# Kernel optimization log

Measured on AMD Instinct MI355X. Metric: run time of the kernel, lower is better.

Reference implementation:

```python
import jax, jax.numpy as jnp
import numpy as np

EMBED = 1024
HEADS = 16
HEAD_DIM = EMBED // HEADS


def setup_inputs() -> dict:
    key = jax.random.key(0)
    k1, k2, k3, k4, k5 = jax.random.split(key, 5)
    x = jax.random.normal(k1, (2, 2048, EMBED), dtype=jnp.float32)
    # torch nn.Linear params: weight [out, in], bias [out]; y = x @ W.T + b
    s_attn = 1.0 / np.sqrt(EMBED)
    w_attn = jax.random.uniform(k2, (3 * EMBED, EMBED), jnp.float32, -s_attn, s_attn)
    b_attn = jax.random.uniform(k3, (3 * EMBED,), jnp.float32, -s_attn, s_attn)
    w_proj = jax.random.uniform(k4, (EMBED, EMBED), jnp.float32, -s_attn, s_attn)
    b_proj = jax.random.uniform(k5, (EMBED,), jnp.float32, -s_attn, s_attn)
    return {"x": x, "w_attn": w_attn, "b_attn": b_attn, "w_proj": w_proj, "b_proj": b_proj}


def reference(x, w_attn, b_attn, w_proj, b_proj):
    B, S, D = x.shape
    qkv = x @ w_attn.T + b_attn                      # [B, S, 3D]
    q, k, v = jnp.split(qkv, 3, axis=-1)             # each [B, S, D]

    def heads(t):  # [B, S, D] -> [B, H, S, hd]
        return t.reshape(B, S, HEADS, HEAD_DIM).transpose(0, 2, 1, 3)

    q, k, v = heads(q), heads(k), heads(v)
    # Faithful to source: NO 1/sqrt(d) scaling, NO causal mask.
    w = jnp.einsum('bhqd,bhkd->bhqk', q, k)          # [B, H, S, S]
    w = jax.nn.softmax(w, axis=-1)
    a = jnp.einsum('bhqk,bhkd->bhqd', w, v)          # [B, H, S, hd]
    a = a.transpose(0, 2, 1, 3).reshape(B, S, D)     # merge heads
    return a @ w_proj.T + b_proj
```

## Files before the change

kernel.cpp:

```cpp
#include <hip/hip_runtime.h>
#include <hip/hip_bf16.h>
#include <stdint.h>
#include <math.h>


typedef __attribute__((ext_vector_type(2))) float f32x2;
typedef __attribute__((ext_vector_type(4))) float f32x4;
typedef __attribute__((ext_vector_type(16))) float f32x16;
typedef __attribute__((ext_vector_type(8))) short bf16x8;

static __device__ __forceinline__ unsigned short f2bf(float f) {
    unsigned u = __float_as_uint(f);
    u += 0x7FFFu + ((u >> 16) & 1u);
    return (unsigned short)(u >> 16);
}
static __device__ __forceinline__ unsigned cvt_pk_bf16(float a, float b) {
    unsigned r;
    asm("v_cvt_pk_bf16_f32 %0, %1, %2" : "=v"(r) : "v"(a), "v"(b));
    return r;
}

typedef const __attribute__((address_space(1))) unsigned int* gas_ptr;
typedef __attribute__((address_space(3))) unsigned int* las_ptr;
static __device__ __forceinline__ void gload_lds16(const void* g, void* l) {
    __builtin_amdgcn_global_load_lds((gas_ptr)g, (las_ptr)l, 16, 0, 0);
}

__global__ void conv_all_kernel(const float* __restrict__ x,
                                const float* __restrict__ wa,
                                const float* __restrict__ wp,
                                unsigned short* __restrict__ x1,
                                unsigned short* __restrict__ w1a,
                                unsigned short* __restrict__ wpb) {
    int i = blockIdx.x * blockDim.x + threadIdx.x;
    int stride = gridDim.x * blockDim.x;
    for (; i < 2097152; i += stride) {
        const float* s; unsigned short* d; int j;
        if (i < 1048576)      { s = x;  d = x1;  j = i; }
        else if (i < 1835008) { s = wa; d = w1a; j = i - 1048576; }
        else                  { s = wp; d = wpb; j = i - 1835008; }
        float4 v = ((const float4*)s)[j];
        ushort4 o;
        o.x = f2bf(v.x); o.y = f2bf(v.y); o.z = f2bf(v.z); o.w = f2bf(v.w);
        ((ushort4*)d)[j] = o;
    }
}

template <int MODE>
__global__ __launch_bounds__(256, 2) void gemm_bt_kernel(
    const unsigned short* __restrict__ A,
    const unsigned short* __restrict__ Bw,
    const float* __restrict__ bias,
    unsigned short* __restrict__ q1,
    unsigned short* __restrict__ k1,
    unsigned short* __restrict__ vT,
    float* __restrict__ outp,
    int N, int K)
{
    __shared__ __align__(16) unsigned char lds[32768];
    const int t  = threadIdx.x;
    const int lane = t & 63;
    const int w  = t >> 6;
    const int wr = w >> 1, wc = w & 1;
    const int lg = lane >> 4, ll = lane & 15;

    const int gx = gridDim.x;
    const int flat = blockIdx.y * gx + blockIdx.x;
    const int cpx = (gx * gridDim.y) >> 3;
    const int swz = (flat & 7) * cpx + (flat >> 3);
    const int m0 = (swz / gx) * 128;
    const int n0 = (swz % gx) * 128;

    f32x4 acc[4][4] = {};

    const int srow  = t >> 3;
    const int sslot = t & 7;
    const unsigned short* Abase[4];
    const unsigned short* Bbase[4];
#pragma unroll
    for (int ci = 0; ci < 4; ++ci) {
        int r  = ci * 32 + srow;
        int cg = sslot ^ (r & 7);
        Abase[ci] = A  + (size_t)(m0 + r) * K + cg * 8;
        Bbase[ci] = Bw + (size_t)(n0 + r) * K + cg * 8;
    }

    for (int k0 = 0; k0 < K; k0 += 64) {
#pragma unroll
        for (int ci = 0; ci < 4; ++ci)
            gload_lds16(Abase[ci] + k0, lds + ci*4096 + (t>>6)*1024);
#pragma unroll
        for (int ci = 0; ci < 4; ++ci)
            gload_lds16(Bbase[ci] + k0, lds + 16384 + ci*4096 + (t>>6)*1024);
        __syncthreads();

        bf16x8 af[4][2], bfr[4][2];
#pragma unroll
        for (int mt = 0; mt < 4; ++mt)
#pragma unroll
            for (int kc = 0; kc < 2; ++kc) {
                int row = wr*64 + mt*16 + ll;
                int cg  = (4*kc + lg) ^ (row & 7);
                af[mt][kc] = *(const bf16x8*)(lds + row*128 + cg*16);
            }
#pragma unroll
        for (int nt = 0; nt < 4; ++nt)
#pragma unroll
            for (int kc = 0; kc < 2; ++kc) {
                int row = wc*64 + nt*16 + ll;
                int cg  = (4*kc + lg) ^ (row & 7);
                bfr[nt][kc] = *(const bf16x8*)(lds + 16384 + row*128 + cg*16);
            }
#pragma unroll
        for (int kc = 0; kc < 2; ++kc)
#pragma unroll
            for (int mt = 0; mt < 4; ++mt)
#pragma unroll
                for (int nt = 0; nt < 4; ++nt)
                    acc[mt][nt] = __builtin_amdgcn_mfma_f32_16x16x32_bf16(
                        af[mt][kc], bfr[nt][kc], acc[mt][nt], 0, 0, 0);
        __syncthreads();
    }

#pragma unroll
    for (int mt = 0; mt < 4; ++mt)
#pragma unroll
      for (int nt = 0; nt < 4; ++nt)
#pragma unroll
        for (int r = 0; r < 4; ++r) {
            int m = m0 + wr*64 + mt*16 + 4*lg + r;
            int n = n0 + wc*64 + nt*16 + ll;
            float v = acc[mt][nt][r] + bias[n];
            if (MODE == 0) {
                int bb = m >> 11;
                int s  = m & 2047;
                int which = n >> 10;
                int h  = (n >> 6) & 15;
                int d  = n & 63;
                int bh = bb * 16 + h;
                if (which == 2) {
                    vT[((size_t)bh * 64 + d) * 2048 + s] = f2bf(v);
                } else {
                    float vq = (which == 0) ? v * 1.44269504f : v;
                    unsigned short* dp = (which == 0 ? q1 : k1)
                                       + ((size_t)bh * 2048 + s) * 64 + d;
                    *dp = f2bf(vq);
                }
            } else {
                outp[(size_t)m * N + n] = v;
            }
        }
}

__global__ __launch_bounds__(512, 4) void attn_kernel(
    const unsigned short* __restrict__ q1,
    const unsigned short* __restrict__ k1,
    const unsigned short* __restrict__ vT,
    unsigned short* __restrict__ aout)
{
    __shared__ __align__(16) unsigned char lds[65536];
    const int t = threadIdx.x, lane = t & 63, w = t >> 6;
    const int hi = lane >> 5, lq = lane & 31, l7 = lane & 7;
    const int gp = w >> 2, sw = w & 3;

    const int D  = blockIdx.x;
    const int bh = (D & 7) + ((D >> 7) << 3);
    const int qb = (D >> 3) & 15;
    const int q0 = qb * 128 + sw * 32;

    bf16x8 qf[4];
    {
        const unsigned short* qp = q1 + ((size_t)bh*2048 + q0 + lq)*64 + hi*8;
#pragma unroll
        for (int ks = 0; ks < 4; ++ks)
            qf[ks] = *(const bf16x8*)(qp + ks*16);
    }

    f32x16 o0 = {}, o1 = {};
    f32x2 lr2 = {0.f, 0.f};
    const f32x16 fz = {};

    const int sr = t >> 3, ss = t & 7;
    const int scg = ss ^ (sr & 7);
    const int psr = (sr & 51) | ((sr & 4) << 1) | ((sr & 8) >> 1);
    const unsigned short* Ksrc = k1 + ((size_t)bh*2048 + psr)*64 + scg*8;
    const unsigned short* Vsrc = vT + ((size_t)bh*64 + sr)*2048 + scg*8;
    const int sdst = w*1024;

    unsigned char* fb0 = lds + gp*8192 + lq*128 + (((0 + hi) ^ l7) << 4);
    unsigned char* fb1 = lds + gp*8192 + lq*128 + (((2 + hi) ^ l7) << 4);
    unsigned char* fb2 = lds + gp*8192 + lq*128 + (((4 + hi) ^ l7) << 4);
    unsigned char* fb3 = lds + gp*8192 + lq*128 + (((6 + hi) ^ l7) << 4);

    gload_lds16(Ksrc,        lds + sdst);
    gload_lds16(Ksrc + 4096, lds + 8192 + sdst);
    gload_lds16(Vsrc,        lds + 32768 + sdst);
    gload_lds16(Vsrc + 64,   lds + 32768 + 8192 + sdst);
    __syncthreads();

#define SOFT_PACK(SV, PA, PB)                                                 \
    {                                                                         \
        float e0 =exp2f(SV[0]),  e1 =exp2f(SV[1]),  e2 =exp2f(SV[2]);         \
        float e3 =exp2f(SV[3]),  e4 =exp2f(SV[4]),  e5 =exp2f(SV[5]);         \
        float e6 =exp2f(SV[6]),  e7 =exp2f(SV[7]),  e8 =exp2f(SV[8]);         \
        float e9 =exp2f(SV[9]),  e10=exp2f(SV[10]), e11=exp2f(SV[11]);        \
        float e12=exp2f(SV[12]), e13=exp2f(SV[13]), e14=exp2f(SV[14]);        \
        float e15=exp2f(SV[15]);                                              \
        union { unsigned u[4]; bf16x8 v; } A_, B_;                            \
        A_.u[0]=cvt_pk_bf16(e0,e1);   A_.u[1]=cvt_pk_bf16(e2,e3);             \
        A_.u[2]=cvt_pk_bf16(e4,e5);   A_.u[3]=cvt_pk_bf16(e6,e7);             \
        B_.u[0]=cvt_pk_bf16(e8,e9);   B_.u[1]=cvt_pk_bf16(e10,e11);           \
        B_.u[2]=cvt_pk_bf16(e12,e13); B_.u[3]=cvt_pk_bf16(e14,e15);           \
        PA = A_.v; PB = B_.v;                                                 \
        f32x2 p0 = {e0,e1};   p0 += (f32x2){e2,e3};                           \
        p0 += (f32x2){e4,e5};   p0 += (f32x2){e6,e7};                         \
        p0 += (f32x2){e8,e9};   p0 += (f32x2){e10,e11};                       \
        p0 += (f32x2){e12,e13}; p0 += (f32x2){e14,e15};                       \
        lr2 += p0;                                                            \
    }

#define ATTN_STEP(PAR)                                                        \
    {                                                                         \
        f32x16 s0, s1;                                                        \
        bf16x8 kf;                                                            \
        __builtin_amdgcn_s_setprio(1);                                        \
        kf = *(const bf16x8*)(fb0 + (PAR)*16384);                             \
        s0 = __builtin_amdgcn_mfma_f32_32x32x16_bf16(kf, qf[0], fz, 0,0,0);   \
        kf = *(const bf16x8*)(fb0 + (PAR)*16384 + 4096);                      \
        s1 = __builtin_amdgcn_mfma_f32_32x32x16_bf16(kf, qf[0], fz, 0,0,0);   \
        kf = *(const bf16x8*)(fb1 + (PAR)*16384);                             \
        s0 = __builtin_amdgcn_mfma_f32_32x32x16_bf16(kf, qf[1], s0, 0,0,0);   \
        kf = *(const bf16x8*)(fb1 + (PAR)*16384 + 4096);                      \
        s1 = __builtin_amdgcn_mfma_f32_32x32x16_bf16(kf, qf[1], s1, 0,0,0);   \
        kf = *(const bf16x8*)(fb2 + (PAR)*16384);                             \
        s0 = __builtin_amdgcn_mfma_f32_32x32x16_bf16(kf, qf[2], s0, 0,0,0);   \
        kf = *(const bf16x8*)(fb2 + (PAR)*16384 + 4096);                      \
        s1 = __builtin_amdgcn_mfma_f32_32x32x16_bf16(kf, qf[2], s1, 0,0,0);   \
        kf = *(const bf16x8*)(fb3 + (PAR)*16384);                             \
        s0 = __builtin_amdgcn_mfma_f32_32x32x16_bf16(kf, qf[3], s0, 0,0,0);   \
        kf = *(const bf16x8*)(fb3 + (PAR)*16384 + 4096);                      \
        s1 = __builtin_amdgcn_mfma_f32_32x32x16_bf16(kf, qf[3], s1, 0,0,0);   \
        __builtin_amdgcn_s_setprio(0);                                        \
        bf16x8 pa0, pa1, pa2, pa3;                                            \
        SOFT_PACK(s0, pa0, pa1)                                               \
        SOFT_PACK(s1, pa2, pa3)                                               \
        bf16x8 vf;                                                            \
        __builtin_amdgcn_s_setprio(1);                                        \
        vf = *(const bf16x8*)(fb0 + (PAR)*16384 + 32768);                     \
        o0 = __builtin_amdgcn_mfma_f32_32x32x16_bf16(pa0, vf, o0, 0,0,0);     \
        vf = *(const bf16x8*)(fb0 + (PAR)*16384 + 32768 + 4096);              \
        o1 = __builtin_amdgcn_mfma_f32_32x32x16_bf16(pa0, vf, o1, 0,0,0);     \
        vf = *(const bf16x8*)(fb1 + (PAR)*16384 + 32768);                     \
        o0 = __builtin_amdgcn_mfma_f32_32x32x16_bf16(pa1, vf, o0, 0,0,0);     \
        vf = *(const bf16x8*)(fb1 + (PAR)*16384 + 32768 + 4096);              \
        o1 = __builtin_amdgcn_mfma_f32_32x32x16_bf16(pa1, vf, o1, 0,0,0);     \
        vf = *(const bf16x8*)(fb2 + (PAR)*16384 + 32768);                     \
        o0 = __builtin_amdgcn_mfma_f32_32x32x16_bf16(pa2, vf, o0, 0,0,0);     \
        vf = *(const bf16x8*)(fb2 + (PAR)*16384 + 32768 + 4096);              \
        o1 = __builtin_amdgcn_mfma_f32_32x32x16_bf16(pa2, vf, o1, 0,0,0);     \
        vf = *(const bf16x8*)(fb3 + (PAR)*16384 + 32768);                     \
        o0 = __builtin_amdgcn_mfma_f32_32x32x16_bf16(pa3, vf, o0, 0,0,0);     \
        vf = *(const bf16x8*)(fb3 + (PAR)*16384 + 32768 + 4096);              \
        o1 = __builtin_amdgcn_mfma_f32_32x32x16_bf16(pa3, vf, o1, 0,0,0);     \
        __builtin_amdgcn_s_setprio(0);                                        \
    }

    for (int sp = 0; sp < 8; ++sp) {
        {
            const size_t T = 4*(size_t)sp + 2;
            gload_lds16(Ksrc + T*4096,        lds + 16384 + sdst);
            gload_lds16(Ksrc + T*4096 + 4096, lds + 24576 + sdst);
            gload_lds16(Vsrc + T*64,          lds + 32768 + 16384 + sdst);
            gload_lds16(Vsrc + T*64 + 64,     lds + 32768 + 24576 + sdst);
            ATTN_STEP(0)
            __syncthreads();
        }
        {
            if (sp < 7) {
                const size_t T = 4*(size_t)sp + 4;
                gload_lds16(Ksrc + T*4096,        lds + sdst);
                gload_lds16(Ksrc + T*4096 + 4096, lds + 8192 + sdst);
                gload_lds16(Vsrc + T*64,          lds + 32768 + sdst);
                gload_lds16(Vsrc + T*64 + 64,     lds + 32768 + 8192 + sdst);
            }
            ATTN_STEP(1)
            __syncthreads();
        }
    }
#undef ATTN_STEP
#undef SOFT_PACK

    float lrow = lr2[0] + lr2[1];
    lrow += __shfl_xor(lrow, 32);

    float* mb = (float*)lds;
    const int slot = (sw << 6) + lane;
    if (gp == 1) {
        float* p = mb + slot * 32;
#pragma unroll
        for (int c = 0; c < 4; ++c) {
            f32x4 v = { o0[4*c], o0[4*c+1], o0[4*c+2], o0[4*c+3] };
            *(f32x4*)(p + 4*c) = v;
        }
#pragma unroll
        for (int c = 0; c < 4; ++c) {
            f32x4 v = { o1[4*c], o1[4*c+1], o1[4*c+2], o1[4*c+3] };
            *(f32x4*)(p + 16 + 4*c) = v;
        }
        mb[8192 + slot] = lrow;
    }
    __syncthreads();
    if (gp == 0) {
        const float* p = mb + slot * 32;
#pragma unroll
        for (int c = 0; c < 4; ++c) {
            f32x4 v = *(const f32x4*)(p + 4*c);
            o0[4*c] += v[0]; o0[4*c+1] += v[1]; o0[4*c+2] += v[2]; o0[4*c+3] += v[3];
        }
#pragma unroll
        for (int c = 0; c < 4; ++c) {
            f32x4 v = *(const f32x4*)(p + 16 + 4*c);
            o1[4*c] += v[0]; o1[4*c+1] += v[1]; o1[4*c+2] += v[2]; o1[4*c+3] += v[3];
        }
        lrow += mb[8192 + slot];

        const int bb = bh >> 4, h = bh & 15;
#pragma unroll
        for (int r = 0; r < 16; ++r) {
            int qrow = (r & 3) + 8*(r >> 2) + 4*hi;
            float linv = 1.0f / __shfl(lrow, qrow);
            size_t srow = q0 + qrow;
            aout[((size_t)(bb*2048 + srow)*16 + h)*64 + lq]      = f2bf(o0[r] * linv);
            aout[((size_t)(bb*2048 + srow)*16 + h)*64 + 32 + lq] = f2bf(o1[r] * linv);
        }
    }
}

extern "C" void kernel_launch(void* const* d_in, const int* in_sizes, int n_in,
                              void* d_out, int out_size, void* d_ws, size_t ws_size,
                              hipStream_t stream) {
    const float* x      = (const float*)d_in[0];
    const float* w_attn = (const float*)d_in[1];
    const float* b_attn = (const float*)d_in[2];
    const float* w_proj = (const float*)d_in[3];
    const float* b_proj = (const float*)d_in[4];
    float* out = (float*)d_out;

    unsigned char* ws = (unsigned char*)d_ws;
    unsigned short* x1  = (unsigned short*)(ws);
    unsigned short* w1a = (unsigned short*)(ws + (size_t)8*1024*1024);
    unsigned short* wpb = (unsigned short*)(ws + (size_t)14*1024*1024);
    unsigned short* q1  = (unsigned short*)(ws + (size_t)16*1024*1024);
    unsigned short* k1  = (unsigned short*)(ws + (size_t)24*1024*1024);
    unsigned short* vT  = (unsigned short*)(ws + (size_t)32*1024*1024);
    unsigned short* ab  = (unsigned short*)(ws + (size_t)40*1024*1024);

    conv_all_kernel<<<2048, 256, 0, stream>>>(x, w_attn, w_proj, x1, w1a, wpb);

    gemm_bt_kernel<0><<<dim3(24, 32), 256, 0, stream>>>(
        x1, w1a, b_attn, q1, k1, vT, nullptr, 3072, 1024);

    attn_kernel<<<512, 512, 0, stream>>>(q1, k1, vT, ab);

    gemm_bt_kernel<1><<<dim3(8, 32), 256, 0, stream>>>(
        ab, wpb, b_proj, nullptr, nullptr, nullptr, out, 1024, 1024);
}
```

Before: 119.7 us.

## Add dedicated 128x64 proj GEMM, raw v_exp in softmax, hoist V LDS loads

The output-projection GEMM gets its own kernel with 128x64 tiles, so it launches 512 blocks instead of 256 and fills more CUs on the small 4096x1024 problem. The attention softmax now calls v_exp_f32 through inline asm instead of exp2f, which skips the library's range-handling wrapper. The V fragment LDS reads are issued before the softmax so their latency overlaps the exp work. In exchange, the proj tiles get less reuse per block, the hoisted loads need more registers, and the raw exp gives up denormal and edge-case handling.

```diff
diff --git a/kernel.cpp b/kernel.cpp
--- a/kernel.cpp
+++ b/kernel.cpp
@@ -17,6 +17,11 @@
 static __device__ __forceinline__ unsigned cvt_pk_bf16(float a, float b) {
     unsigned r;
     asm("v_cvt_pk_bf16_f32 %0, %1, %2" : "=v"(r) : "v"(a), "v"(b));
+    return r;
+}
+static __device__ __forceinline__ float fexp2(float x) {
+    float r;
+    asm("v_exp_f32 %0, %1" : "=v"(r) : "v"(x));
     return r;
 }
 
@@ -46,15 +51,13 @@
     }
 }
 
-template <int MODE>
-__global__ __launch_bounds__(256, 2) void gemm_bt_kernel(
+__global__ __launch_bounds__(256, 2) void gemm_qkv_kernel(
     const unsigned short* __restrict__ A,
     const unsigned short* __restrict__ Bw,
     const float* __restrict__ bias,
     unsigned short* __restrict__ q1,
     unsigned short* __restrict__ k1,
     unsigned short* __restrict__ vT,
-    float* __restrict__ outp,
     int N, int K)
 {
     __shared__ __align__(16) unsigned char lds[32768];
@@ -131,24 +134,105 @@
             int m = m0 + wr*64 + mt*16 + 4*lg + r;
             int n = n0 + wc*64 + nt*16 + ll;
             float v = acc[mt][nt][r] + bias[n];
-            if (MODE == 0) {
-                int bb = m >> 11;
-                int s  = m & 2047;
-                int which = n >> 10;
-                int h  = (n >> 6) & 15;
-                int d  = n & 63;
-                int bh = bb * 16 + h;
-                if (which == 2) {
-                    vT[((size_t)bh * 64 + d) * 2048 + s] = f2bf(v);
-                } else {
-                    float vq = (which == 0) ? v * 1.44269504f : v;
-                    unsigned short* dp = (which == 0 ? q1 : k1)
-                                       + ((size_t)bh * 2048 + s) * 64 + d;
-                    *dp = f2bf(vq);
-                }
+            int bb = m >> 11;
+            int s  = m & 2047;
+            int which = n >> 10;
+            int h  = (n >> 6) & 15;
+            int d  = n & 63;
+            int bh = bb * 16 + h;
+            if (which == 2) {
+                vT[((size_t)bh * 64 + d) * 2048 + s] = f2bf(v);
             } else {
-                outp[(size_t)m * N + n] = v;
-            }
+                float vq = (which == 0) ? v * 1.44269504f : v;
+                unsigned short* dp = (which == 0 ? q1 : k1)
+                                   + ((size_t)bh * 2048 + s) * 64 + d;
+                *dp = f2bf(vq);
+            }
+        }
+}
+
+__global__ __launch_bounds__(256, 2) void gemm_proj_kernel(
+    const unsigned short* __restrict__ A,
+    const unsigned short* __restrict__ Bw,
+    const float* __restrict__ bias,
+    float* __restrict__ outp)
+{
+    __shared__ __align__(16) unsigned char lds[24576];
+    const int t  = threadIdx.x;
+    const int lane = t & 63;
+    const int w  = t >> 6;
+    const int lg = lane >> 4, ll = lane & 15;
+
+    const int flat = blockIdx.y * 16 + blockIdx.x;
+    const int swz = (flat & 7) * 64 + (flat >> 3);
+    const int m0 = (swz >> 4) * 128;
+    const int n0 = (swz & 15) * 64;
+
+    f32x4 acc[2][4] = {};
+
+    const int srow  = t >> 3;
+    const int sslot = t & 7;
+    const unsigned short* Abase[4];
+    const unsigned short* Bbase[2];
+#pragma unroll
+    for (int ci = 0; ci < 4; ++ci) {
+        int r  = ci * 32 + srow;
+        int cg = sslot ^ (r & 7);
+        Abase[ci] = A + (size_t)(m0 + r) * 1024 + cg * 8;
+    }
+#pragma unroll
+    for (int ci = 0; ci < 2; ++ci) {
+        int r  = ci * 32 + srow;
+        int cg = sslot ^ (r & 7);
+        Bbase[ci] = Bw + (size_t)(n0 + r) * 1024 + cg * 8;
+    }
+
+    for (int k0 = 0; k0 < 1024; k0 += 64) {
+#pragma unroll
+        for (int ci = 0; ci < 4; ++ci)
+            gload_lds16(Abase[ci] + k0, lds + ci*4096 + w*1024);
+#pragma unroll
+        for (int ci = 0; ci < 2; ++ci)
+            gload_lds16(Bbase[ci] + k0, lds + 16384 + ci*4096 + w*1024);
+        __syncthreads();
+
+        bf16x8 af[2][2], bfr[4][2];
+#pragma unroll
+        for (int mt = 0; mt < 2; ++mt)
+#pragma unroll
+            for (int kc = 0; kc < 2; ++kc) {
+                int row = w*32 + mt*16 + ll;
+                int cg  = (4*kc + lg) ^ (row & 7);
+                af[mt][kc] = *(const bf16x8*)(lds + row*128 + cg*16);
+            }
+#pragma unroll
+        for (int nt = 0; nt < 4; ++nt)
+#pragma unroll
+            for (int kc = 0; kc < 2; ++kc) {
+                int row = nt*16 + ll;
+                int cg  = (4*kc + lg) ^ (row & 7);
+                bfr[nt][kc] = *(const bf16x8*)(lds + 16384 + row*128 + cg*16);
+            }
+#pragma unroll
+        for (int kc = 0; kc < 2; ++kc)
+#pragma unroll
+            for (int mt = 0; mt < 2; ++mt)
+#pragma unroll
+                for (int nt = 0; nt < 4; ++nt)
+                    acc[mt][nt] = __builtin_amdgcn_mfma_f32_16x16x32_bf16(
+                        af[mt][kc], bfr[nt][kc], acc[mt][nt], 0, 0, 0);
+        __syncthreads();
+    }
+
+#pragma unroll
+    for (int mt = 0; mt < 2; ++mt)
+#pragma unroll
+      for (int nt = 0; nt < 4; ++nt)
+#pragma unroll
+        for (int r = 0; r < 4; ++r) {
+            int m = m0 + w*32 + mt*16 + 4*lg + r;
+            int n = n0 + nt*16 + ll;
+            outp[(size_t)m * 1024 + n] = acc[mt][nt][r] + bias[n];
         }
 }
 
@@ -200,12 +284,12 @@
 
 #define SOFT_PACK(SV, PA, PB)                                                 \
     {                                                                         \
-        float e0 =exp2f(SV[0]),  e1 =exp2f(SV[1]),  e2 =exp2f(SV[2]);         \
-        float e3 =exp2f(SV[3]),  e4 =exp2f(SV[4]),  e5 =exp2f(SV[5]);         \
-        float e6 =exp2f(SV[6]),  e7 =exp2f(SV[7]),  e8 =exp2f(SV[8]);         \
-        float e9 =exp2f(SV[9]),  e10=exp2f(SV[10]), e11=exp2f(SV[11]);        \
-        float e12=exp2f(SV[12]), e13=exp2f(SV[13]), e14=exp2f(SV[14]);        \
-        float e15=exp2f(SV[15]);                                              \
+        float e0 =fexp2(SV[0]),  e1 =fexp2(SV[1]),  e2 =fexp2(SV[2]);         \
+        float e3 =fexp2(SV[3]),  e4 =fexp2(SV[4]),  e5 =fexp2(SV[5]);         \
+        float e6 =fexp2(SV[6]),  e7 =fexp2(SV[7]),  e8 =fexp2(SV[8]);         \
+        float e9 =fexp2(SV[9]),  e10=fexp2(SV[10]), e11=fexp2(SV[11]);        \
+        float e12=fexp2(SV[12]), e13=fexp2(SV[13]), e14=fexp2(SV[14]);        \
+        float e15=fexp2(SV[15]);                                              \
         union { unsigned u[4]; bf16x8 v; } A_, B_;                            \
         A_.u[0]=cvt_pk_bf16(e0,e1);   A_.u[1]=cvt_pk_bf16(e2,e3);             \
         A_.u[2]=cvt_pk_bf16(e4,e5);   A_.u[3]=cvt_pk_bf16(e6,e7);             \
@@ -241,27 +325,27 @@
         kf = *(const bf16x8*)(fb3 + (PAR)*16384 + 4096);                      \
         s1 = __builtin_amdgcn_mfma_f32_32x32x16_bf16(kf, qf[3], s1, 0,0,0);   \
         __builtin_amdgcn_s_setprio(0);                                        \
+                 \
+        bf16x8 v00 = *(const bf16x8*)(fb0 + (PAR)*16384 + 32768);             \
+        bf16x8 v01 = *(const bf16x8*)(fb0 + (PAR)*16384 + 32768 + 4096);      \
+        bf16x8 v10 = *(const bf16x8*)(fb1 + (PAR)*16384 + 32768);             \
+        bf16x8 v11 = *(const bf16x8*)(fb1 + (PAR)*16384 + 32768 + 4096);      \
+        bf16x8 v20 = *(const bf16x8*)(fb2 + (PAR)*16384 + 32768);             \
+        bf16x8 v21 = *(const bf16x8*)(fb2 + (PAR)*16384 + 32768 + 4096);      \
+        bf16x8 v30 = *(const bf16x8*)(fb3 + (PAR)*16384 + 32768);             \
+        bf16x8 v31 = *(const bf16x8*)(fb3 + (PAR)*16384 + 32768 + 4096);      \
         bf16x8 pa0, pa1, pa2, pa3;                                            \
         SOFT_PACK(s0, pa0, pa1)                                               \
         SOFT_PACK(s1, pa2, pa3)                                               \
-        bf16x8 vf;                                                            \
         __builtin_amdgcn_s_setprio(1);                                        \
-        vf = *(const bf16x8*)(fb0 + (PAR)*16384 + 32768);                     \
-        o0 = __builtin_amdgcn_mfma_f32_32x32x16_bf16(pa0, vf, o0, 0,0,0);     \
-        vf = *(const bf16x8*)(fb0 + (PAR)*16384 + 32768 + 4096);              \
-        o1 = __builtin_amdgcn_mfma_f32_32x32x16_bf16(pa0, vf, o1, 0,0,0);     \
-        vf = *(const bf16x8*)(fb1 + (PAR)*16384 + 32768);                     \
-        o0 = __builtin_amdgcn_mfma_f32_32x32x16_bf16(pa1, vf, o0, 0,0,0);     \
-        vf = *(const bf16x8*)(fb1 + (PAR)*16384 + 32768 + 4096);              \
-        o1 = __builtin_amdgcn_mfma_f32_32x32x16_bf16(pa1, vf, o1, 0,0,0);     \
-        vf = *(const bf16x8*)(fb2 + (PAR)*16384 + 32768);                     \
-        o0 = __builtin_amdgcn_mfma_f32_32x32x16_bf16(pa2, vf, o0, 0,0,0);     \
-        vf = *(const bf16x8*)(fb2 + (PAR)*16384 + 32768 + 4096);              \
-        o1 = __builtin_amdgcn_mfma_f32_32x32x16_bf16(pa2, vf, o1, 0,0,0);     \
-        vf = *(const bf16x8*)(fb3 + (PAR)*16384 + 32768);                     \
-        o0 = __builtin_amdgcn_mfma_f32_32x32x16_bf16(pa3, vf, o0, 0,0,0);     \
-        vf = *(const bf16x8*)(fb3 + (PAR)*16384 + 32768 + 4096);              \
-        o1 = __builtin_amdgcn_mfma_f32_32x32x16_bf16(pa3, vf, o1, 0,0,0);     \
+        o0 = __builtin_amdgcn_mfma_f32_32x32x16_bf16(pa0, v00, o0, 0,0,0);    \
+        o1 = __builtin_amdgcn_mfma_f32_32x32x16_bf16(pa0, v01, o1, 0,0,0);    \
+        o0 = __builtin_amdgcn_mfma_f32_32x32x16_bf16(pa1, v10, o0, 0,0,0);    \
+        o1 = __builtin_amdgcn_mfma_f32_32x32x16_bf16(pa1, v11, o1, 0,0,0);    \
+        o0 = __builtin_amdgcn_mfma_f32_32x32x16_bf16(pa2, v20, o0, 0,0,0);    \
+        o1 = __builtin_amdgcn_mfma_f32_32x32x16_bf16(pa2, v21, o1, 0,0,0);    \
+        o0 = __builtin_amdgcn_mfma_f32_32x32x16_bf16(pa3, v30, o0, 0,0,0);    \
+        o1 = __builtin_amdgcn_mfma_f32_32x32x16_bf16(pa3, v31, o1, 0,0,0);    \
         __builtin_amdgcn_s_setprio(0);                                        \
     }
 
@@ -357,11 +441,10 @@
 
     conv_all_kernel<<<2048, 256, 0, stream>>>(x, w_attn, w_proj, x1, w1a, wpb);
 
-    gemm_bt_kernel<0><<<dim3(24, 32), 256, 0, stream>>>(
-        x1, w1a, b_attn, q1, k1, vT, nullptr, 3072, 1024);
+    gemm_qkv_kernel<<<dim3(24, 32), 256, 0, stream>>>(
+        x1, w1a, b_attn, q1, k1, vT, 3072, 1024);
 
     attn_kernel<<<512, 512, 0, stream>>>(q1, k1, vT, ab);
 
-    gemm_bt_kernel<1><<<dim3(8, 32), 256, 0, stream>>>(
-        ab, wpb, b_proj, nullptr, nullptr, nullptr, out, 1024, 1024);
-}
+    gemm_proj_kernel<<<dim3(16, 32), 256, 0, stream>>>(ab, wpb, b_proj, out);
+}
```

Measured after the change: 121.8 us. No clear change (+1.7%).
